# Performance work log

Hardware: AMD Instinct MI355X
Metric: run time of the kernel (lower is better)

The kernel has to match this reference:

```python
import jax, jax.numpy as jnp
import numpy as np
from jax import lax


def _c1x1(t, w, b=None):
    # t: [B,C,H,W], w: [O,C] (1x1 conv == channel matmul)
    y = jnp.einsum('bchw,oc->bohw', t, w)
    if b is not None:
        y = y + b[None, :, None, None]
    return y


def _mamba(u, in_w, conv_w, conv_b, xproj_w, dt_w, dt_b, A_log, Dp, out_w):
    # u: [B,L,d_model]; Mamba block (mamba_ssm defaults: in/out/x_proj bias=False)
    B, L, _ = u.shape
    d_inner = conv_w.shape[0]
    d_state = A_log.shape[1]
    dt_rank = dt_w.shape[1]
    d_conv = conv_w.shape[2]
    xz = jnp.einsum('bld,ed->ble', u, in_w)          # [B,L,2*d_inner]
    xc, z = xz[..., :d_inner], xz[..., d_inner:]
    # depthwise causal conv1d over seq
    xt = jnp.pad(xc.transpose(0, 2, 1), ((0, 0), (0, 0), (d_conv - 1, 0)))
    xt = lax.conv_general_dilated(xt, conv_w, (1,), 'VALID',
                                  feature_group_count=d_inner,
                                  dimension_numbers=('NCH', 'OIH', 'NCH'))
    xc = jax.nn.silu(xt + conv_b[None, :, None]).transpose(0, 2, 1)  # [B,L,d_inner]
    dbc = jnp.einsum('bld,ed->ble', xc, xproj_w)     # [B,L,dt_rank+2*d_state]
    dt = dbc[..., :dt_rank]
    B_ = dbc[..., dt_rank:dt_rank + d_state]
    C_ = dbc[..., dt_rank + d_state:]
    delta = jax.nn.softplus(jnp.einsum('blr,dr->bld', dt, dt_w) + dt_b)  # [B,L,d_inner]
    A = -jnp.exp(A_log)                              # [d_inner,d_state]
    dA = jnp.exp(delta[..., None] * A)               # [B,L,D,N]
    dBu = delta[..., None] * B_[:, :, None, :] * xc[..., None]
    def step(h, inp):
        dA_t, dBu_t, c_t = inp
        h = dA_t * h + dBu_t                         # [B,D,N]
        y = jnp.einsum('bdn,bn->bd', h, c_t)
        return h, y
    h0 = jnp.zeros((B, d_inner, d_state), dtype=u.dtype)
    _, ys = lax.scan(step, h0, (dA.transpose(1, 0, 2, 3),
                                dBu.transpose(1, 0, 2, 3),
                                C_.transpose(1, 0, 2)))
    y = ys.transpose(1, 0, 2) + xc * Dp              # [B,L,d_inner]
    y = y * jax.nn.silu(z)
    return jnp.einsum('bld,od->blo', y, out_w)       # [B,L,d_model]


def setup_inputs() -> dict:
    key = jax.random.key(0)
    B, C, H, W = 8, 128, 160, 160
    mip, d_in, d_st, d_r, d_cv = 8, 256, 16, 8, 4
    ks = iter(jax.random.split(key, 64))
    def rn(shape, s=0.05):
        return (jax.random.normal(next(ks), shape, dtype=jnp.float32) * s)
    inp = {'x': jax.random.normal(next(ks), (B, C, H, W), dtype=jnp.float32)}
    inp.update(conv1_w=rn((mip, C)), conv1_b=rn((mip,)),
               bn_g=jnp.ones((mip,)), bn_b=jnp.zeros((mip,)),
               bn_m=jnp.zeros((mip,)), bn_v=jnp.ones((mip,)),
               convh_w=rn((C, mip)), convh_b=rn((C,)),
               convw_w=rn((C, mip)), convw_b=rn((C,)),
               mlpx_w1=rn((C, C)), mlpx_b1=rn((C,)), mlpx_w2=rn((C, C)), mlpx_b2=rn((C,)),
               mlpy_w1=rn((C, C)), mlpy_b1=rn((C,)), mlpy_w2=rn((C, C)), mlpy_b2=rn((C,)),
               adjust_w=rn((C, 2 * C)))
    for p in ('mx', 'my'):
        inp[p + '_in_w'] = rn((2 * d_in, C))
        inp[p + '_conv_w'] = rn((d_in, 1, d_cv), 0.3)
        inp[p + '_conv_b'] = rn((d_in,))
        inp[p + '_xproj_w'] = rn((d_r + 2 * d_st, d_in))
        inp[p + '_dt_w'] = rn((d_in, d_r))
        inp[p + '_dt_b'] = rn((d_in,))
        inp[p + '_Alog'] = jnp.log(jnp.broadcast_to(jnp.arange(1, d_st + 1, dtype=jnp.float32), (d_in, d_st)))
        inp[p + '_D'] = jnp.ones((d_in,))
        inp[p + '_out_w'] = rn((C, d_in))
    return inp


def reference(x, conv1_w, conv1_b, bn_g, bn_b, bn_m, bn_v, convh_w, convh_b,
              convw_w, convw_b, mlpx_w1, mlpx_b1, mlpx_w2, mlpx_b2,
              mlpy_w1, mlpy_b1, mlpy_w2, mlpy_b2, adjust_w,
              mx_in_w, mx_conv_w, mx_conv_b, mx_xproj_w, mx_dt_w, mx_dt_b,
              mx_Alog, mx_D, mx_out_w,
              my_in_w, my_conv_w, my_conv_b, my_xproj_w, my_dt_w, my_dt_b,
              my_Alog, my_D, my_out_w):
    B, C, H, W = x.shape
    gelu = lambda t: jax.nn.gelu(t, approximate=False)
    # CoordAttWithMLP
    x_h = x.mean(3, keepdims=True)                      # [B,C,H,1]
    x_w = x.mean(2, keepdims=True).transpose(0, 1, 3, 2)  # [B,C,W,1]
    y = jnp.concatenate([x_h, x_w], axis=2)             # [B,C,H+W,1]
    y = _c1x1(y, conv1_w, conv1_b)
    y = (y - bn_m[None, :, None, None]) * jax.lax.rsqrt(bn_v + 1e-5)[None, :, None, None]
    y = y * bn_g[None, :, None, None] + bn_b[None, :, None, None]
    y = gelu(y)
    a_h = _c1x1(y[:, :, :H], convh_w, convh_b)          # [B,C,H,1] (pre-sigmoid)
    a_w = _c1x1(y[:, :, H:].transpose(0, 1, 3, 2), convw_w, convw_b)  # [B,C,1,W]
    # EfficientMambaAttention00
    ux = x.mean(3).transpose(0, 2, 1)                   # [B,H,C]
    x_x = _mamba(ux, mx_in_w, mx_conv_w, mx_conv_b, mx_xproj_w,
                 mx_dt_w, mx_dt_b, mx_Alog, mx_D, mx_out_w)
    x_x = x_x.transpose(0, 2, 1)[..., None]             # [B,C,H,1]
    x_x = jax.nn.sigmoid(x_x + a_h)
    x_x = _c1x1(gelu(_c1x1(x_x, mlpx_w1, mlpx_b1)), mlpx_w2, mlpx_b2)
    uy = x.mean(2).transpose(0, 2, 1)                   # [B,W,C]
    x_y = _mamba(uy, my_in_w, my_conv_w, my_conv_b, my_xproj_w,
                 my_dt_w, my_dt_b, my_Alog, my_D, my_out_w)
    x_y = x_y.transpose(0, 2, 1)[:, :, None, :]         # [B,C,1,W]
    x_y = jax.nn.sigmoid(x_y + a_w)
    x_y = _c1x1(gelu(_c1x1(x_y, mlpy_w1, mlpy_b1)), mlpy_w2, mlpy_b2)
    # combine
    result_h = jax.nn.sigmoid(a_h) * x_y                # [B,C,H,W]
    result_w = jax.nn.sigmoid(a_w) * x_x                # [B,C,H,W]
    out1 = _c1x1(jnp.concatenate([result_h, result_w], axis=1), adjust_w)
    return x * out1
```

## Files before the change

### kernel.cpp

```cpp
#include <hip/hip_runtime.h>
#include <hip/hip_bf16.h>
#include <math.h>


typedef __attribute__((ext_vector_type(8))) short short8;
typedef __attribute__((ext_vector_type(4))) float f32x4;

__device__ __forceinline__ float sigm_(float x){ return 1.f/(1.f+__expf(-x)); }
__device__ __forceinline__ float silu_(float x){ return x/(1.f+__expf(-x)); }
__device__ __forceinline__ float gelu_(float x){ return 0.5f*x*(1.f+erff(x*0.7071067811865476f)); }
__device__ __forceinline__ float softplus_(float x){ return (x>20.f)?x:log1pf(__expf(x)); }

__global__ void k_means(const float* __restrict__ x, float* __restrict__ xh, float* __restrict__ xw){
  int bc = blockIdx.x;
  const float* xt = x + (size_t)bc*25600;
  int tid = threadIdx.x, wave = tid>>6, lane = tid&63;
  __shared__ float4 colpart[4][40];
  float csx=0.f, csy=0.f, csz=0.f, csw=0.f;
  for (int i=0;i<40;i++){
    int h = wave*40+i;
    float4 v = make_float4(0.f,0.f,0.f,0.f);
    if (lane<40) v = ((const float4*)(xt + h*160))[lane];
    csx+=v.x; csy+=v.y; csz+=v.z; csw+=v.w;
    float r = v.x+v.y+v.z+v.w;
    for (int off=32; off>0; off>>=1) r += __shfl_down(r, off, 64);
    if (lane==0) xh[(size_t)bc*160+h] = r*(1.f/160.f);
  }
  if (lane<40) colpart[wave][lane] = make_float4(csx,csy,csz,csw);
  __syncthreads();
  if (tid<40){
    float4 a=colpart[0][tid], b=colpart[1][tid], c=colpart[2][tid], d=colpart[3][tid];
    float4 s = make_float4((a.x+b.x+c.x+d.x)*(1.f/160.f), (a.y+b.y+c.y+d.y)*(1.f/160.f),
                           (a.z+b.z+c.z+d.z)*(1.f/160.f), (a.w+b.w+c.w+d.w)*(1.f/160.f));
    ((float4*)(xw + (size_t)bc*160))[tid] = s;
  }
}

__global__ void k_ybranch(const float* __restrict__ xh, const float* __restrict__ xw,
                          const float* __restrict__ w1, const float* __restrict__ b1,
                          const float* __restrict__ bg, const float* __restrict__ bb,
                          const float* __restrict__ bm, const float* __restrict__ bv,
                          float* __restrict__ ybuf){
  int gid = blockIdx.x*blockDim.x + threadIdx.x;
  if (gid >= 8*320) return;
  int b = gid/320, p = gid%320;
  const float* in = (p<160) ? (xh + (size_t)b*128*160 + p) : (xw + (size_t)b*128*160 + (p-160));
  float acc[8] = {0,0,0,0,0,0,0,0};
  for (int c=0;c<128;c++){
    float u = in[c*160];
    #pragma unroll
    for (int m=0;m<8;m++) acc[m] += w1[m*128+c]*u;
  }
  #pragma unroll
  for (int m=0;m<8;m++){
    float val = acc[m] + b1[m];
    val = (val - bm[m]) * rsqrtf(bv[m] + 1e-5f);
    val = val * bg[m] + bb[m];
    ybuf[(b*320+p)*8+m] = gelu_(val);
  }
}

__global__ void k_ahw(const float* __restrict__ ybuf,
                      const float* __restrict__ wh, const float* __restrict__ bh,
                      const float* __restrict__ ww, const float* __restrict__ bw,
                      float* __restrict__ a_h, float* __restrict__ a_w,
                      float* __restrict__ SHT, float* __restrict__ SW,
                      const float* __restrict__ adjw, __hip_bfloat16* __restrict__ adjwb){
  int blk = blockIdx.x;
  if (blk >= 1280){
    int i = (blk-1280)*256 + threadIdx.x;
    if (i < 32768) adjwb[i] = __float2bfloat16(adjw[i]);
    return;
  }
  int gid = blk*256 + threadIdx.x;
  int p = gid%320; int c = (gid/320)%128; int b = gid/(320*128);
  const float* yv = ybuf + (size_t)(b*320+p)*8;
  const float* w = (p<160)? (wh + c*8) : (ww + c*8);
  float acc = (p<160)? bh[c] : bw[c];
  #pragma unroll
  for (int m=0;m<8;m++) acc += w[m]*yv[m];
  if (p<160){
    size_t o = ((size_t)(b*128+c))*160+p;
    a_h[o] = acc;
    SHT[((size_t)(b*160+p))*128 + c] = sigm_(acc);
  } else {
    size_t o = ((size_t)(b*128+c))*160+(p-160);
    a_w[o] = acc; SW[o] = sigm_(acc);
  }
}

__global__ __launch_bounds__(256) void k_inproj(
                         const float* __restrict__ xh, const float* __restrict__ xw,
                         const float* __restrict__ inw0, const float* __restrict__ inw1,
                         float* __restrict__ xcpre, float* __restrict__ zb){
  __shared__ float uS[8][128];
  int blk = blockIdx.x;
  int g = blk/160, rem = blk%160, b = rem/20, lt = rem%20, lbase = lt*8;
  int t = threadIdx.x;
  const float* src = (g==0)? xh : xw;
  {
    int c = t>>1, lh = t&1;
    float4 v = *(const float4*)(src + ((size_t)(b*128+c))*160 + lbase + lh*4);
    uS[lh*4+0][c]=v.x; uS[lh*4+1][c]=v.y; uS[lh*4+2][c]=v.z; uS[lh*4+3][c]=v.w;
  }
  __syncthreads();
  const float* inw = (g==0)? inw0 : inw1;
  const float* w0p = inw + (size_t)t*128;
  const float* w1p = inw + (size_t)(t+256)*128;
  float acc0[8]={0,0,0,0,0,0,0,0}, acc1[8]={0,0,0,0,0,0,0,0};
  for (int ct=0; ct<16; ct++){
    float4 wa = *(const float4*)(w0p + ct*8);
    float4 wb = *(const float4*)(w0p + ct*8 + 4);
    float4 wc = *(const float4*)(w1p + ct*8);
    float4 wd = *(const float4*)(w1p + ct*8 + 4);
    #pragma unroll
    for (int l=0;l<8;l++){
      float4 ua = *(const float4*)&uS[l][ct*8];
      float4 ub = *(const float4*)&uS[l][ct*8+4];
      acc0[l] += wa.x*ua.x + wa.y*ua.y + wa.z*ua.z + wa.w*ua.w
               + wb.x*ub.x + wb.y*ub.y + wb.z*ub.z + wb.w*ub.w;
      acc1[l] += wc.x*ua.x + wc.y*ua.y + wc.z*ua.z + wc.w*ua.w
               + wd.x*ub.x + wd.y*ub.y + wd.z*ub.z + wd.w*ub.w;
    }
  }
  size_t ob = ((size_t)(g*8+b)*160 + lbase)*256;
  #pragma unroll
  for (int l=0;l<8;l++){
    xcpre[ob + (size_t)l*256 + t] = acc0[l];
    zb   [ob + (size_t)l*256 + t] = acc1[l];
  }
}

__global__ void k_conv(const float* __restrict__ xcpre,
                       const float* __restrict__ cw0, const float* __restrict__ cb0,
                       const float* __restrict__ cw1, const float* __restrict__ cb1,
                       float* __restrict__ xcb){
  int gid = blockIdx.x*blockDim.x + threadIdx.x;
  if (gid >= 2*8*160*256) return;
  int d = gid & 255; int t = gid >> 8; int l = t % 160; int gb = t / 160; int g = gb >> 3;
  const float* cw = ((g==0)? cw0 : cw1) + d*4;
  float acc = ((g==0)? cb0 : cb1)[d];
  const float* base = xcpre + (size_t)gb*160*256 + d;
  #pragma unroll
  for (int k=0;k<4;k++){
    int ls = l-3+k;
    if (ls>=0) acc += cw[k] * base[(size_t)ls*256];
  }
  xcb[gid] = silu_(acc);
}

__global__ __launch_bounds__(256) void k_xproj(
                        const float* __restrict__ xcb,
                        const float* __restrict__ xp0, const float* __restrict__ xp1,
                        float* __restrict__ dbc){
  __shared__ float xv[32][260];
  int blk = blockIdx.x;
  int g = blk/40, rem = blk%40, b = rem/5, lt = rem%5, lbase = lt*32;
  int t = threadIdx.x;
  size_t base = ((size_t)(g*8+b)*160 + lbase)*256;
  for (int i=t; i<8192; i+=256){ int l=i>>8, d=i&255; xv[l][d] = xcb[base+i]; }
  __syncthreads();
  int l = t>>3, s = t&7;
  const float* xp = (g==0)? xp0 : xp1;
  size_t orow = ((size_t)(g*8+b)*160 + lbase + l)*40;
  for (int q=0;q<5;q++){
    int j = s + q*8;
    const float* w = xp + j*256;
    float acc=0.f;
    for (int dd=0; dd<256; dd+=8){
      float4 wa = *(const float4*)(w+dd);
      float4 wb = *(const float4*)(w+dd+4);
      float4 ua = *(const float4*)&xv[l][dd];
      float4 ub = *(const float4*)&xv[l][dd+4];
      acc += wa.x*ua.x + wa.y*ua.y + wa.z*ua.z + wa.w*ua.w
           + wb.x*ub.x + wb.y*ub.y + wb.z*ub.z + wb.w*ub.w;
    }
    dbc[orow + j] = acc;
  }
}

__global__ __launch_bounds__(256) void k_scan(
                       const float* __restrict__ dbc,
                       const float* __restrict__ xcb, const float* __restrict__ zb,
                       const float* __restrict__ dtw0, const float* __restrict__ dtb0,
                       const float* __restrict__ dtw1, const float* __restrict__ dtb1,
                       const float* __restrict__ Alog0, const float* __restrict__ Alog1,
                       const float* __restrict__ D0, const float* __restrict__ D1,
                       float* __restrict__ ysb){
  __shared__ float dsS[160][16];
  __shared__ float BS [160][16];
  __shared__ float CS [160][16];
  __shared__ float xcS[160][16];
  __shared__ float yS [160][16];
  int blk = blockIdx.x;
  int gb = blk >> 4, dblk = blk & 15, g = gb >> 3;
  int dbase = dblk*16;
  int t = threadIdx.x;
  size_t base = (size_t)gb*160*256;
  const float* db = dbc + (size_t)gb*6400;
  const float* dtwG = (g==0)? dtw0 : dtw1;
  const float* dtbG = (g==0)? dtb0 : dtb1;

  #pragma unroll
  for (int i=0;i<10;i++){
    int item = t + 256*i;
    int l = item>>4, c = item&15;
    const float* r = db + l*40;
    int d = dbase + c;
    const float* wt = dtwG + d*8;
    float4 w0 = *(const float4*)wt;
    float4 w1 = *(const float4*)(wt+4);
    float4 r0 = *(const float4*)r;
    float4 r1 = *(const float4*)(r+4);
    float dt = dtbG[d] + w0.x*r0.x+w0.y*r0.y+w0.z*r0.z+w0.w*r0.w
                       + w1.x*r1.x+w1.y*r1.y+w1.z*r1.z+w1.w*r1.w;
    dsS[l][c] = softplus_(dt);
    BS [l][c] = r[8+c];
    CS [l][c] = r[24+c];
    xcS[l][c] = xcb[base + (size_t)l*256 + dbase + c];
  }
  __syncthreads();

  int dloc = t>>4, n = t&15;
  int d = dbase + dloc;
  float A  = -__expf(((g==0)? Alog0 : Alog1)[d*16+n]);
  float Dd = ((g==0)? D0 : D1)[d];
  float h = 0.f;
  for (int lc=0; lc<160; lc+=8){
    float ds8[8], B8[8], C8[8], xc8[8];
    #pragma unroll
    for (int j=0;j<8;j++){
      ds8[j]=dsS[lc+j][dloc]; B8[j]=BS[lc+j][n];
      C8[j]=CS[lc+j][n];      xc8[j]=xcS[lc+j][dloc];
    }
    #pragma unroll
    for (int j=0;j<8;j++){
      float dA = __expf(ds8[j]*A);
      h = dA*h + ds8[j]*B8[j]*xc8[j];
      float p = h*C8[j];
      p += __shfl_xor(p,1,16); p += __shfl_xor(p,2,16);
      p += __shfl_xor(p,4,16); p += __shfl_xor(p,8,16);
      if (n==0) yS[lc+j][dloc] = p + xc8[j]*Dd;
    }
  }
  __syncthreads();

  #pragma unroll
  for (int i=0;i<10;i++){
    int item = t + 256*i;
    int l = item>>4, c = item&15;
    size_t gi = base + (size_t)l*256 + dbase + c;
    ysb[gi] = yS[l][c] * silu_(zb[gi]);
  }
}

__global__ __launch_bounds__(256) void k_post(
                       const float* __restrict__ ysb,
                       const float* __restrict__ ow0, const float* __restrict__ ow1,
                       const float* __restrict__ a_h, const float* __restrict__ a_w,
                       const float* __restrict__ w1x, const float* __restrict__ b1x,
                       const float* __restrict__ w1y, const float* __restrict__ b1y,
                       const float* __restrict__ w2x, const float* __restrict__ b2x,
                       const float* __restrict__ w2y, const float* __restrict__ b2y,
                       float* __restrict__ QxT, float* __restrict__ Qy){
  __shared__ float ysS[10][256];
  __shared__ float Sc[10][128];
  __shared__ float Sp[10][128];
  int blk = blockIdx.x;
  int g = blk>>7, rem = blk&127, b = rem>>4, lt = rem&15, lbase = lt*10;
  int t = threadIdx.x; int c = t&127, kh = t>>7;
  size_t ybase = ((size_t)(g*8+b)*160 + lbase)*256;
  for (int i=t; i<2560; i+=256) ((float*)ysS)[i] = ysb[ybase+i];
  __syncthreads();
  float acc[10];
  {
    const float* w = ((g==0)? ow0 : ow1) + (size_t)c*256 + kh*128;
    #pragma unroll
    for (int l=0;l<10;l++) acc[l]=0.f;
    for (int ct=0; ct<16; ct++){
      float4 wa = *(const float4*)(w + ct*8);
      float4 wb = *(const float4*)(w + ct*8 + 4);
      #pragma unroll
      for (int l=0;l<10;l++){
        float4 ua = *(const float4*)&ysS[l][kh*128+ct*8];
        float4 ub = *(const float4*)&ysS[l][kh*128+ct*8+4];
        acc[l] += wa.x*ua.x + wa.y*ua.y + wa.z*ua.z + wa.w*ua.w
                + wb.x*ub.x + wb.y*ub.y + wb.z*ub.z + wb.w*ub.w;
      }
    }
  }
  if (kh==1){ for (int l=0;l<10;l++) Sc[l][c] = acc[l]; }
  __syncthreads();
  if (kh==0){
    const float* a = ((g==0)? a_h : a_w) + ((size_t)(b*128+c))*160 + lbase;
    #pragma unroll
    for (int l=0;l<10;l++) Sp[l][c] = sigm_(acc[l] + Sc[l][c] + a[l]);
  }
  __syncthreads();
  {
    const float* w = ((g==0)? w1x : w1y) + (size_t)c*128 + kh*64;
    #pragma unroll
    for (int l=0;l<10;l++) acc[l]=0.f;
    for (int ct=0; ct<8; ct++){
      float4 wa = *(const float4*)(w + ct*8);
      float4 wb = *(const float4*)(w + ct*8 + 4);
      #pragma unroll
      for (int l=0;l<10;l++){
        float4 ua = *(const float4*)&Sp[l][kh*64+ct*8];
        float4 ub = *(const float4*)&Sp[l][kh*64+ct*8+4];
        acc[l] += wa.x*ua.x + wa.y*ua.y + wa.z*ua.z + wa.w*ua.w
                + wb.x*ub.x + wb.y*ub.y + wb.z*ub.z + wb.w*ub.w;
      }
    }
  }
  if (kh==1){ for (int l=0;l<10;l++) Sc[l][c] = acc[l]; }
  __syncthreads();
  if (kh==0){
    float bb = ((g==0)? b1x : b1y)[c];
    float tv[10];
    #pragma unroll
    for (int l=0;l<10;l++) tv[l] = gelu_(bb + acc[l] + Sc[l][c]);
    __syncthreads();
    #pragma unroll
    for (int l=0;l<10;l++) Sp[l][c] = tv[l];
  } else {
    __syncthreads();
  }
  __syncthreads();
  {
    const float* w = ((g==0)? w2x : w2y) + (size_t)c*128 + kh*64;
    #pragma unroll
    for (int l=0;l<10;l++) acc[l]=0.f;
    for (int ct=0; ct<8; ct++){
      float4 wa = *(const float4*)(w + ct*8);
      float4 wb = *(const float4*)(w + ct*8 + 4);
      #pragma unroll
      for (int l=0;l<10;l++){
        float4 ua = *(const float4*)&Sp[l][kh*64+ct*8];
        float4 ub = *(const float4*)&Sp[l][kh*64+ct*8+4];
        acc[l] += wa.x*ua.x + wa.y*ua.y + wa.z*ua.z + wa.w*ua.w
                + wb.x*ub.x + wb.y*ub.y + wb.z*ub.z + wb.w*ub.w;
      }
    }
  }
  if (kh==1){ for (int l=0;l<10;l++) Sc[l][c] = acc[l]; }
  __syncthreads();
  if (kh==0){
    float bb = ((g==0)? b2x : b2y)[c];
    if (g==0){
      #pragma unroll
      for (int l=0;l<10;l++)
        QxT[((size_t)(b*160 + lbase + l))*128 + c] = bb + acc[l] + Sc[l][c];
    } else {
      size_t orow = ((size_t)(b*128+c))*160 + lbase;
      #pragma unroll
      for (int l=0;l<10;l++) Qy[orow + l] = bb + acc[l] + Sc[l][c];
    }
  }
}

__device__ __forceinline__ void build_F(__hip_bfloat16* Fb, float s, const float4* v,
                                        int whh, int kq){
  #pragma unroll
  for (int u=0;u<10;u++){
    int wr = whh*40 + u*4;
    Fb[(wr+0)*136 + kq] = __float2bfloat16(s*v[u].x);
    Fb[(wr+1)*136 + kq] = __float2bfloat16(s*v[u].y);
    Fb[(wr+2)*136 + kq] = __float2bfloat16(s*v[u].z);
    Fb[(wr+3)*136 + kq] = __float2bfloat16(s*v[u].w);
  }
}

__global__ __launch_bounds__(256,2) void k_final_mfma(
                       const float* __restrict__ x,
                       const float* __restrict__ SHT, const float* __restrict__ SW,
                       const float* __restrict__ QxT, const float* __restrict__ Qy,
                       const __hip_bfloat16* __restrict__ adjwb, float* __restrict__ out){
  __shared__ __hip_bfloat16 F[2][80*136];
  int blk0 = blockIdx.x;
  int b = blk0 & 7, inner = blk0 >> 3;
  int ht = inner >> 1, wh = inner & 1;
  int h0 = ht*5;
  int wbase = wh*80;
  int tid = threadIdx.x;
  int kq = tid & 127, whh = tid >> 7;
  int wid = tid>>6, lane = tid&63, quad = lane>>4, l16 = lane&15;

  float s0[5], s1[5];
  #pragma unroll
  for (int j=0;j<5;j++){
    s0[j] = SHT[((size_t)(b*160+h0+j))*128 + kq];
    s1[j] = QxT[((size_t)(b*160+h0+j))*128 + kq];
  }
  size_t prow = ((size_t)(b*128+kq))*160 + wbase + whh*40;
  const float4* rp0 = (const float4*)(Qy + prow);
  const float4* rp1 = (const float4*)(SW + prow);
  float4 v0[10], v1[10];
  #pragma unroll
  for (int u=0;u<10;u++) v0[u] = rp0[u];
  #pragma unroll
  for (int u=0;u<10;u++) v1[u] = rp1[u];

  build_F(F[0], s0[0], v0, whh, kq);
  __syncthreads();

  size_t rowA = ((size_t)(b*128 + (wid*2+0)*16 + l16))*25600 + wbase + quad*4;
  size_t rowB = ((size_t)(b*128 + (wid*2+1)*16 + l16))*25600 + wbase + quad*4;

  #pragma unroll
  for (int j=0;j<5;j++){
    int h = h0 + j;
    float4 xv[2][5];
    #pragma unroll
    for (int nt=0;nt<5;nt++){
      xv[0][nt] = *(const float4*)(x + rowA + (size_t)h*160 + nt*16);
      xv[1][nt] = *(const float4*)(x + rowB + (size_t)h*160 + nt*16);
    }
    f32x4 acc[2][5];
    #pragma unroll
    for (int i=0;i<2;i++)
      #pragma unroll
      for (int nt=0;nt<5;nt++) acc[i][nt] = (f32x4){0.f,0.f,0.f,0.f};

    {
      short8 bf[2][4];
      #pragma unroll
      for (int i=0;i<2;i++){
        const __hip_bfloat16* bp = adjwb + (size_t)((wid*2+i)*16 + l16)*256 + quad*8;
        #pragma unroll
        for (int kc=0;kc<4;kc++) bf[i][kc] = *(const short8*)(bp + kc*32);
      }
      #pragma unroll
      for (int nt=0; nt<5; nt++){
        const __hip_bfloat16* ap = &F[0][(nt*16 + l16)*136 + quad*8];
        #pragma unroll
        for (int kc=0;kc<4;kc++){
          short8 af = *(const short8*)(ap + kc*32);
          acc[0][nt] = __builtin_amdgcn_mfma_f32_16x16x32_bf16(af, bf[0][kc], acc[0][nt], 0,0,0);
          acc[1][nt] = __builtin_amdgcn_mfma_f32_16x16x32_bf16(af, bf[1][kc], acc[1][nt], 0,0,0);
        }
      }
    }
    build_F(F[1], s1[j], v1, whh, kq);
    __syncthreads();

    {
      short8 bf[2][4];
      #pragma unroll
      for (int i=0;i<2;i++){
        const __hip_bfloat16* bp = adjwb + (size_t)((wid*2+i)*16 + l16)*256 + 128 + quad*8;
        #pragma unroll
        for (int kc=0;kc<4;kc++) bf[i][kc] = *(const short8*)(bp + kc*32);
      }
      #pragma unroll
      for (int nt=0; nt<5; nt++){
        const __hip_bfloat16* ap = &F[1][(nt*16 + l16)*136 + quad*8];
        #pragma unroll
        for (int kc=0;kc<4;kc++){
          short8 af = *(const short8*)(ap + kc*32);
          acc[0][nt] = __builtin_amdgcn_mfma_f32_16x16x32_bf16(af, bf[0][kc], acc[0][nt], 0,0,0);
          acc[1][nt] = __builtin_amdgcn_mfma_f32_16x16x32_bf16(af, bf[1][kc], acc[1][nt], 0,0,0);
        }
      }
    }
    if (j<4) build_F(F[0], s0[j+1], v0, whh, kq);

    #pragma unroll
    for (int i=0;i<2;i++){
      size_t rb = (i? rowB : rowA) + (size_t)h*160;
      #pragma unroll
      for (int nt=0; nt<5; nt++){
        f32x4 a = acc[i][nt];
        float4 xvv = xv[i][nt];
        float4 ov = make_float4(xvv.x*a[0], xvv.y*a[1], xvv.z*a[2], xvv.w*a[3]);
        *(float4*)(out + rb + nt*16) = ov;
      }
    }
    __syncthreads();
  }
}

extern "C" void kernel_launch(void* const* d_in, const int* in_sizes, int n_in,
                              void* d_out, int out_size, void* d_ws, size_t ws_size,
                              hipStream_t stream) {
  #define W(i) ((const float*)d_in[i])
  const float* X = W(0);
  float* ws = (float*)d_ws;
  float* xh    = ws;
  float* xw    = xh    + 163840;
  float* ybuf  = xw    + 163840;
  float* ah    = ybuf  + 20480;
  float* aw    = ah    + 163840;
  float* xcpre = aw    + 163840;
  float* zb    = xcpre + 655360;
  float* xcb   = zb    + 655360;
  float* dbc   = xcb   + 655360;
  float* ysb   = dbc   + 102400;
  float* QxT   = ysb   + 655360;
  float* Qy    = QxT   + 163840;
  __hip_bfloat16* adjwb = (__hip_bfloat16*)xcpre;
  float* SHT   = xcpre + 16384;
  float* SW    = SHT   + 163840;

  k_means  <<<1024, 256, 0, stream>>>(X, xh, xw);
  k_ybranch<<<10,   256, 0, stream>>>(xh, xw, W(1), W(2), W(3), W(4), W(5), W(6), ybuf);
  k_inproj <<<320,  256, 0, stream>>>(xh, xw, W(20), W(29), xcpre, zb);
  k_conv   <<<2560, 256, 0, stream>>>(xcpre, W(21), W(22), W(30), W(31), xcb);
  k_ahw    <<<1408, 256, 0, stream>>>(ybuf, W(7), W(8), W(9), W(10), ah, aw, SHT, SW,
                                      W(19), adjwb);
  k_xproj  <<<80,   256, 0, stream>>>(xcb, W(23), W(32), dbc);
  k_scan   <<<256,  256, 0, stream>>>(dbc, xcb, zb, W(24), W(25), W(33), W(34),
                                      W(26), W(35), W(27), W(36), ysb);
  k_post   <<<256,  256, 0, stream>>>(ysb, W(28), W(37), ah, aw,
                                      W(11), W(12), W(15), W(16),
                                      W(13), W(14), W(17), W(18), QxT, Qy);
  k_final_mfma<<<512, 256, 0, stream>>>(X, SHT, SW, QxT, Qy, adjwb, (float*)d_out);
  #undef W
}
```

Baseline: 458.1 us.

## Shrink final MFMA tile to 32 columns and raise occupancy with lighter barriers

The final fused adjust-conv kernel now tiles W into five 32-wide chunks instead of two 80-wide halves. This raises the grid from 512 to 1280 blocks and cuts LDS and register use so four blocks per CU can be resident. Block-wide __syncthreads is replaced by an explicit LDS waitcnt plus s_barrier, so the barrier no longer waits on outstanding global stores. The cost is that each block reuses its weight fragments over fewer columns and reloads per-channel scalars more often.

```diff
diff --git a/kernel.cpp b/kernel.cpp
--- a/kernel.cpp
+++ b/kernel.cpp
@@ -5,6 +5,9 @@
 
 typedef __attribute__((ext_vector_type(8))) short short8;
 typedef __attribute__((ext_vector_type(4))) float f32x4;
+
+#define LDS_BARRIER() do { asm volatile("s_waitcnt lgkmcnt(0)" ::: "memory"); \
+                           __builtin_amdgcn_s_barrier(); } while(0)
 
 __device__ __forceinline__ float sigm_(float x){ return 1.f/(1.f+__expf(-x)); }
 __device__ __forceinline__ float silu_(float x){ return x/(1.f+__expf(-x)); }
@@ -360,10 +363,10 @@
 }
 
 __device__ __forceinline__ void build_F(__hip_bfloat16* Fb, float s, const float4* v,
-                                        int whh, int kq){
-  #pragma unroll
-  for (int u=0;u<10;u++){
-    int wr = whh*40 + u*4;
+                                        int wg, int kq){
+  #pragma unroll
+  for (int u=0;u<4;u++){
+    int wr = wg*16 + u*4;
     Fb[(wr+0)*136 + kq] = __float2bfloat16(s*v[u].x);
     Fb[(wr+1)*136 + kq] = __float2bfloat16(s*v[u].y);
     Fb[(wr+2)*136 + kq] = __float2bfloat16(s*v[u].z);
@@ -371,19 +374,19 @@
   }
 }
 
-__global__ __launch_bounds__(256,2) void k_final_mfma(
+__global__ __launch_bounds__(256,4) void k_final_mfma(
                        const float* __restrict__ x,
                        const float* __restrict__ SHT, const float* __restrict__ SW,
                        const float* __restrict__ QxT, const float* __restrict__ Qy,
                        const __hip_bfloat16* __restrict__ adjwb, float* __restrict__ out){
-  __shared__ __hip_bfloat16 F[2][80*136];
+  __shared__ __hip_bfloat16 F[2][32*136];
   int blk0 = blockIdx.x;
   int b = blk0 & 7, inner = blk0 >> 3;
-  int ht = inner >> 1, wh = inner & 1;
+  int ht = inner/5, wq = inner%5;
   int h0 = ht*5;
-  int wbase = wh*80;
+  int wbase = wq*32;
   int tid = threadIdx.x;
-  int kq = tid & 127, whh = tid >> 7;
+  int kq = tid & 127, wg = tid >> 7;
   int wid = tid>>6, lane = tid&63, quad = lane>>4, l16 = lane&15;
 
   float s0[5], s1[5];
@@ -392,46 +395,46 @@
     s0[j] = SHT[((size_t)(b*160+h0+j))*128 + kq];
     s1[j] = QxT[((size_t)(b*160+h0+j))*128 + kq];
   }
-  size_t prow = ((size_t)(b*128+kq))*160 + wbase + whh*40;
+  size_t prow = ((size_t)(b*128+kq))*160 + wbase + wg*16;
   const float4* rp0 = (const float4*)(Qy + prow);
   const float4* rp1 = (const float4*)(SW + prow);
-  float4 v0[10], v1[10];
-  #pragma unroll
-  for (int u=0;u<10;u++) v0[u] = rp0[u];
-  #pragma unroll
-  for (int u=0;u<10;u++) v1[u] = rp1[u];
-
-  build_F(F[0], s0[0], v0, whh, kq);
-  __syncthreads();
-
-  size_t rowA = ((size_t)(b*128 + (wid*2+0)*16 + l16))*25600 + wbase + quad*4;
-  size_t rowB = ((size_t)(b*128 + (wid*2+1)*16 + l16))*25600 + wbase + quad*4;
+  float4 v0[4], v1[4];
+  #pragma unroll
+  for (int u=0;u<4;u++) v0[u] = rp0[u];
+  #pragma unroll
+  for (int u=0;u<4;u++) v1[u] = rp1[u];
+
+  build_F(F[0], s0[0], v0, wg, kq);
+  LDS_BARRIER();
+
+  size_t rowA = ((size_t)(b*128 + wid*32 + l16))*25600 + wbase + quad*4;
+  size_t rowB = rowA + (size_t)16*25600;
 
   #pragma unroll
   for (int j=0;j<5;j++){
     int h = h0 + j;
-    float4 xv[2][5];
-    #pragma unroll
-    for (int nt=0;nt<5;nt++){
+    float4 xv[2][2];
+    #pragma unroll
+    for (int nt=0;nt<2;nt++){
       xv[0][nt] = *(const float4*)(x + rowA + (size_t)h*160 + nt*16);
       xv[1][nt] = *(const float4*)(x + rowB + (size_t)h*160 + nt*16);
     }
-    f32x4 acc[2][5];
+    f32x4 acc[2][2];
     #pragma unroll
     for (int i=0;i<2;i++)
       #pragma unroll
-      for (int nt=0;nt<5;nt++) acc[i][nt] = (f32x4){0.f,0.f,0.f,0.f};
+      for (int nt=0;nt<2;nt++) acc[i][nt] = (f32x4){0.f,0.f,0.f,0.f};
 
     {
       short8 bf[2][4];
       #pragma unroll
       for (int i=0;i<2;i++){
-        const __hip_bfloat16* bp = adjwb + (size_t)((wid*2+i)*16 + l16)*256 + quad*8;
+        const __hip_bfloat16* bp = adjwb + (size_t)(wid*32 + i*16 + l16)*256 + quad*8;
         #pragma unroll
         for (int kc=0;kc<4;kc++) bf[i][kc] = *(const short8*)(bp + kc*32);
       }
       #pragma unroll
-      for (int nt=0; nt<5; nt++){
+      for (int nt=0; nt<2; nt++){
         const __hip_bfloat16* ap = &F[0][(nt*16 + l16)*136 + quad*8];
         #pragma unroll
         for (int kc=0;kc<4;kc++){
@@ -441,19 +444,19 @@
         }
       }
     }
-    build_F(F[1], s1[j], v1, whh, kq);
-    __syncthreads();
+    build_F(F[1], s1[j], v1, wg, kq);
+    LDS_BARRIER();
 
     {
       short8 bf[2][4];
       #pragma unroll
       for (int i=0;i<2;i++){
-        const __hip_bfloat16* bp = adjwb + (size_t)((wid*2+i)*16 + l16)*256 + 128 + quad*8;
+        const __hip_bfloat16* bp = adjwb + (size_t)(wid*32 + i*16 + l16)*256 + 128 + quad*8;
         #pragma unroll
         for (int kc=0;kc<4;kc++) bf[i][kc] = *(const short8*)(bp + kc*32);
       }
       #pragma unroll
-      for (int nt=0; nt<5; nt++){
+      for (int nt=0; nt<2; nt++){
         const __hip_bfloat16* ap = &F[1][(nt*16 + l16)*136 + quad*8];
         #pragma unroll
         for (int kc=0;kc<4;kc++){
@@ -463,20 +466,20 @@
         }
       }
     }
-    if (j<4) build_F(F[0], s0[j+1], v0, whh, kq);
+    if (j<4) build_F(F[0], s0[j+1], v0, wg, kq);
 
     #pragma unroll
     for (int i=0;i<2;i++){
       size_t rb = (i? rowB : rowA) + (size_t)h*160;
       #pragma unroll
-      for (int nt=0; nt<5; nt++){
+      for (int nt=0; nt<2; nt++){
         f32x4 a = acc[i][nt];
         float4 xvv = xv[i][nt];
         float4 ov = make_float4(xvv.x*a[0], xvv.y*a[1], xvv.z*a[2], xvv.w*a[3]);
         *(float4*)(out + rb + nt*16) = ov;
       }
     }
-    __syncthreads();
+    LDS_BARRIER();
   }
 }
 
@@ -514,6 +517,6 @@
   k_post   <<<256,  256, 0, stream>>>(ysb, W(28), W(37), ah, aw,
                                       W(11), W(12), W(15), W(16),
                                       W(13), W(14), W(17), W(18), QxT, Qy);
-  k_final_mfma<<<512, 256, 0, stream>>>(X, SHT, SW, QxT, Qy, adjwb, (float*)d_out);
+  k_final_mfma<<<1280, 256, 0, stream>>>(X, SHT, SW, QxT, Qy, adjwb, (float*)d_out);
   #undef W
 }
```

Result: no change. 463.9 us (+1.3%).
